# Performance work log

Hardware: AMD Instinct MI355X
Metric: run time of the kernel (lower is better)

The kernel has to match this reference:

```python
import jax, jax.numpy as jnp
import numpy as np

B, T, C, H = 4, 2048, 1024, 16
D = C // H  # head_dim = 64


def setup_inputs() -> dict:
    key = jax.random.key(0)
    ks = jax.random.split(key, 4)
    scale = 1.0 / np.sqrt(C)
    return {
        "x": jax.random.normal(ks[0], (B, T, C), dtype=jnp.float32),
        "attn_mask": jnp.ones((B, T), dtype=jnp.int32),
        "W_qkv": jax.random.normal(ks[1], (C, 3 * C), dtype=jnp.float32) * scale,
        "b_qkv": jnp.zeros((3 * C,), dtype=jnp.float32),
        "W_proj": jax.random.normal(ks[2], (C, C), dtype=jnp.float32) * scale,
        "b_proj": jnp.zeros((C,), dtype=jnp.float32),
    }


def reference(x, attn_mask, W_qkv, b_qkv, W_proj, b_proj):
    b, t, c = x.shape
    qkv = x @ W_qkv + b_qkv                      # (B,T,3C)
    q, k, v = jnp.split(qkv, 3, axis=-1)
    # b t (h d) -> b h t d
    q = q.reshape(b, t, H, D).transpose(0, 2, 1, 3)
    k = k.reshape(b, t, H, D).transpose(0, 2, 1, 3)
    v = v.reshape(b, t, H, D).transpose(0, 2, 1, 3)
    att = jnp.einsum("bhtd,bhsd->bhts", q, k) / jnp.sqrt(jnp.float32(D))
    causal = jnp.tril(jnp.ones((t, t), dtype=bool))[None, None]       # (1,1,T,T)
    pad = (attn_mask[:, None, None, :t] != 0)                         # (B,1,1,T)
    att = jnp.where(causal & pad, att, -jnp.inf)
    att = jax.nn.softmax(att, axis=-1)
    y = jnp.einsum("bhts,bhsd->bhtd", att, v)   # (B,H,T,D)
    y = y.transpose(0, 2, 1, 3).reshape(b, t, c)
    return y @ W_proj + b_proj
```

## Files before the change

kernel.cpp:

```cpp
#include <hip/hip_runtime.h>
#include <math.h>

#define B_ 4
#define T_ 2048
#define C_ 1024
#define H_ 16
#define D_ 64
#define M_ (B_*T_)
#define N1_ (3*C_)

typedef __attribute__((ext_vector_type(8))) short bf16x8;
typedef __attribute__((ext_vector_type(4))) short bf16x4;
typedef __attribute__((ext_vector_type(4))) float f32x4;
typedef __attribute__((ext_vector_type(16))) float f32x16;

__device__ __forceinline__ short f2bf(float f){
  union { float f; unsigned u; } v; v.f = f;
  unsigned r = (v.u + 0x7fffu + ((v.u >> 16) & 1u)) >> 16;
  return (short)r;
}

__device__ __forceinline__ unsigned cvtpk(float lo, float hi){
  unsigned r;
  asm("v_cvt_pk_bf16_f32 %0, %1, %2" : "=v"(r) : "v"(lo), "v"(hi));
  return r;
}

__device__ __forceinline__ void plswap(unsigned &a, unsigned &b){
  asm volatile("v_permlane32_swap_b32 %0, %1" : "+v"(a), "+v"(b));
}
__device__ __forceinline__ float xhalf_add(float x){
  unsigned a = __float_as_uint(x), b = a;
  asm volatile("v_permlane32_swap_b32 %0, %1" : "+v"(a), "+v"(b));
  return __uint_as_float(a) + __uint_as_float(b);
}

__device__ __forceinline__ void gll16(const void* g, void* l){
  __builtin_amdgcn_global_load_lds((const __attribute__((address_space(1))) void*)g,
                                   (__attribute__((address_space(3))) void*)l, 16, 0, 0);
}

__global__ __launch_bounds__(256) void convx(const float* __restrict__ x, short* __restrict__ xb, int n){
  int i = (blockIdx.x*256 + threadIdx.x)*8;
  if (i >= n) return;
  float4 a = *(const float4*)(x+i), b = *(const float4*)(x+i+4);
  bf16x8 o;
  o[0]=f2bf(a.x); o[1]=f2bf(a.y); o[2]=f2bf(a.z); o[3]=f2bf(a.w);
  o[4]=f2bf(b.x); o[5]=f2bf(b.y); o[6]=f2bf(b.z); o[7]=f2bf(b.w);
  *(bf16x8*)(xb+i) = o;
}

__global__ __launch_bounds__(256) void transw(const float* __restrict__ W, short* __restrict__ Wt, int K, int N){
  __shared__ float tl[64][72];
  int tid = threadIdx.x;
  int n0 = blockIdx.x*64, k0 = blockIdx.y*64;
  #pragma unroll
  for (int i=0;i<4;i++){
    int row = (tid>>4) + i*16;
    int col4 = (tid&15)*4;
    float4 v = *(const float4*)&W[(size_t)(k0+row)*N + n0 + col4];
    *(float4*)&tl[row][col4] = v;
  }
  __syncthreads();
  #pragma unroll
  for (int i=0;i<2;i++){
    int nr = (tid>>3) + i*32;
    int ch = tid&7;
    bf16x8 o;
    #pragma unroll
    for (int e=0;e<8;e++) o[e] = f2bf(tl[ch*8+e][nr]);
    *(bf16x8*)&Wt[(size_t)(n0+nr)*K + k0 + ch*8] = o;
  }
}

template<int OUTBF>
__global__ __launch_bounds__(512) void gemm_bt(const short* __restrict__ A, const short* __restrict__ Bt,
           const float* __restrict__ bias, short* __restrict__ outb, float* __restrict__ outf,
           int M, int N, int K)
{
  __shared__ __attribute__((aligned(128))) char LDSC[147456];
  const int tid = threadIdx.x;
  const int wv = tid>>6, ln = tid&63;
  const int lnr = ln&15, lg = ln>>4;
  const int wm = wv>>1, wn = wv&1;
  const int nx = gridDim.x;
  const int nwg = nx*gridDim.y;
  const int lin = blockIdx.x + nx*blockIdx.y;
  const int swz = (lin&7)*(nwg>>3) + (lin>>3);
  const int m0 = (swz/nx)*256, n0 = (swz%nx)*128;

  const int srA = tid>>3;
  const int sg  = (tid&7) ^ (srA&7);
  const short* Ag = A  + (size_t)(m0 + srA)*K + sg*8;
  const short* Bg = Bt + (size_t)(n0 + srA)*K + sg*8;

  const int fsw = (lg ^ (lnr&7))<<4;
  const int aln = (wm*64 + lnr)*128 + fsw;
  const int bln = (wn*64 + lnr)*128 + fsw;

  auto STAGE = [&](int kt, int bi){
    const short* a = Ag + kt*64;
    const short* b = Bg + kt*64;
    char* ab = LDSC + bi*32768 + wv*1024;
    char* bb = LDSC + 98304 + bi*16384 + wv*1024;
    gll16(a,                ab);
    gll16(a + (size_t)64*K, ab + 8192);
    gll16(a + (size_t)128*K, ab + 16384);
    gll16(a + (size_t)192*K, ab + 24576);
    gll16(b,                bb);
    gll16(b + (size_t)64*K, bb + 8192);
  };

  f32x4 acc[4][4];
  #pragma unroll
  for (int i=0;i<4;i++)
    #pragma unroll
    for (int j=0;j<4;j++) acc[i][j] = (f32x4){0.f,0.f,0.f,0.f};

  const int NT = K >> 6;
  STAGE(0, 0);
  STAGE(1, 1);
  asm volatile("s_waitcnt vmcnt(6)" ::: "memory");
  __builtin_amdgcn_sched_barrier(0);
  __builtin_amdgcn_s_barrier();
  __builtin_amdgcn_sched_barrier(0);

  int cb = 0, sb = 2;
  #pragma unroll 1
  for (int kt = 0; kt < NT; kt++){
    if (kt + 2 < NT) STAGE(kt + 2, sb);

    const char* ab = LDSC + cb*32768;
    const char* bb = LDSC + 98304 + cb*16384;
    bf16x8 af[4][2], bfr[4][2];
    #pragma unroll
    for (int mi=0;mi<4;mi++)
      #pragma unroll
      for (int ks=0;ks<2;ks++)
        af[mi][ks] = *(const bf16x8*)(ab + ((aln + mi*2048) ^ (ks<<6)));
    #pragma unroll
    for (int ni=0;ni<4;ni++)
      #pragma unroll
      for (int ks=0;ks<2;ks++)
        bfr[ni][ks] = *(const bf16x8*)(bb + ((bln + ni*2048) ^ (ks<<6)));

    __builtin_amdgcn_s_setprio(1);
    #pragma unroll
    for (int mi=0;mi<4;mi++)
      #pragma unroll
      for (int ni=0;ni<4;ni++)
        #pragma unroll
        for (int ks=0;ks<2;ks++)
          acc[mi][ni] = __builtin_amdgcn_mfma_f32_16x16x32_bf16(af[mi][ks], bfr[ni][ks], acc[mi][ni], 0,0,0);
    __builtin_amdgcn_s_setprio(0);

    if (kt < NT-1){
      __builtin_amdgcn_sched_barrier(0);
      if (kt < NT-2){ asm volatile("s_waitcnt vmcnt(6)" ::: "memory"); }
      else          { asm volatile("s_waitcnt vmcnt(0)" ::: "memory"); }
      __builtin_amdgcn_sched_barrier(0);
      __builtin_amdgcn_s_barrier();
      __builtin_amdgcn_sched_barrier(0);
    }
    cb = (cb==2) ? 0 : cb+1;
    sb = (sb==2) ? 0 : sb+1;
  }

  #pragma unroll
  for (int mi=0;mi<4;mi++){
    #pragma unroll
    for (int ni=0;ni<4;ni++){
      int col = n0 + wn*64 + ni*16 + lnr;
      float bv = bias[col];
      #pragma unroll
      for (int r=0;r<4;r++){
        int row = m0 + wm*64 + mi*16 + lg*4 + r;
        float v = acc[mi][ni][r] + bv;
        if (OUTBF) outb[(size_t)row*N + col] = f2bf(v);
        else       outf[(size_t)row*N + col] = v;
      }
    }
  }
}

__global__ __launch_bounds__(256) void transv(const short* __restrict__ qkv, short* __restrict__ vt){
  __shared__ short tl[64][72];
  int tid = threadIdx.x;
  int t0 = blockIdx.x*64, bh = blockIdx.y;
  int b = bh>>4, h = bh&15;
  int tr = tid>>2, cc = (tid&3)*16;
  const short* src = &qkv[(size_t)(b*T_ + t0 + tr)*N1_ + 2*C_ + h*D_ + cc];
  #pragma unroll
  for (int i=0;i<4;i++){
    bf16x4 v = *(const bf16x4*)(src + i*4);
    *(bf16x4*)&tl[tr][cc + i*4] = v;
  }
  __syncthreads();
  int d = tid>>2, tc = (tid&3)*16;
  #pragma unroll
  for (int i=0;i<2;i++){
    bf16x8 o;
    #pragma unroll
    for (int e=0;e<8;e++) o[e] = tl[tc + i*8 + e][d];
    *(bf16x8*)&vt[(size_t)(bh*D_ + d)*T_ + t0 + tc + i*8] = o;
  }
}

__global__ __launch_bounds__(256) void attn12(const short* __restrict__ qkv, const short* __restrict__ vt,
           const int* __restrict__ mask, short* __restrict__ yb)
{
  __shared__ short Ks[64*64];
  __shared__ short Vs[64*64];
  const int tid = threadIdx.x;
  const int wv = tid>>6, ln = tid&63;
  const int l31 = ln & 31, hi = ln >> 5;
  const int bh = blockIdx.x, b = bh>>4, hd = bh&15;
  const int c = 15 - (int)blockIdx.y;
  const float cexp = 0.18033688f;
  const float MC   = 11.541561f;

  const int srow = tid>>3;
  const int scol = (tid&7) ^ (srow&7);
  const short* kgb = qkv + (size_t)(b*T_ + srow)*N1_ + C_ + hd*D_ + scol*8;
  const short* vgb = vt  + (size_t)((bh<<6) + srow)*T_ + scol*8;
  int fa[4];
  #pragma unroll
  for (int i=0;i<4;i++)
    fa[i] = l31*128 + ((((i<<1)+hi) ^ (l31&7)) << 4);

  char* ksb = (char*)Ks;
  char* vsb = (char*)Vs;

  const int q0w = c*128 + wv*32;
  const int ntb  = 2*c + 2;
  const int myNt = 2*c + 1 + (wv>>1);

  bf16x8 qf[4];
  const short* qbase = qkv + (size_t)(b*T_ + q0w + l31)*N1_ + hd*D_ + hi*8;
  #pragma unroll
  for (int ds=0; ds<4; ds++) qf[ds] = *(const bf16x8*)(qbase + ds*16);

  f32x16 o0, o1;
  #pragma unroll
  for (int r=0;r<16;r++){ o0[r]=0.f; o1[r]=0.f; }
  float lsum = 0.f;

  #pragma unroll 1
  for (int jt = 0; jt < ntb; jt++){
    const int j0 = jt << 6;

    int mval = mask[b*T_ + j0 + ln];
    const short* kg = kgb + (size_t)j0*N1_;
    const short* vg = vgb + j0;
    gll16(kg,                    ksb + wv*1024);
    gll16(kg + (size_t)32*N1_,   ksb + 4096 + wv*1024);
    gll16(vg,                    vsb + wv*1024);
    gll16(vg + (size_t)32*T_,    vsb + 4096 + wv*1024);
    unsigned long long bm = __ballot(mval != 0);
    __syncthreads();

    if (jt < myNt){
      f32x16 s0, s1;
      #pragma unroll
      for (int r=0;r<16;r++){ s0[r]=0.f; s1[r]=0.f; }
      __builtin_amdgcn_s_setprio(1);
      #pragma unroll
      for (int ds=0; ds<4; ds++){
        bf16x8 k0 = *(const bf16x8*)(ksb + fa[ds]);
        bf16x8 k1 = *(const bf16x8*)(ksb + fa[ds] + 4096);
        s0 = __builtin_amdgcn_mfma_f32_32x32x16_bf16(k0, qf[ds], s0, 0,0,0);
        s1 = __builtin_amdgcn_mfma_f32_32x32x16_bf16(k1, qf[ds], s1, 0,0,0);
      }
      __builtin_amdgcn_s_setprio(0);

      const int qglob = q0w + l31;
      const bool allm = (bm == ~0ull);
      if (!allm){
        #pragma unroll
        for (int r=0;r<16;r++){
          int kr = (r&3) + 8*(r>>2) + 4*hi;
          bool ok0 = (j0 + kr      <= qglob) && ((bm >> kr) & 1);
          bool ok1 = (j0 + kr + 32 <= qglob) && ((bm >> (kr+32)) & 1);
          s0[r] = ok0 ? s0[r] : -INFINITY;
          s1[r] = ok1 ? s1[r] : -INFINITY;
        }
      } else if (j0 + 63 > q0w){
        #pragma unroll
        for (int r=0;r<16;r++){
          int kr = (r&3) + 8*(r>>2) + 4*hi;
          s0[r] = (j0 + kr      <= qglob) ? s0[r] : -INFINITY;
          s1[r] = (j0 + kr + 32 <= qglob) ? s1[r] : -INFINITY;
        }
      }

      #pragma unroll
      for (int r=0;r<16;r++){
        s0[r] = __builtin_amdgcn_exp2f(__builtin_fmaf(s0[r], cexp, -MC));
        s1[r] = __builtin_amdgcn_exp2f(__builtin_fmaf(s1[r], cexp, -MC));
      }
      float u[8];
      #pragma unroll
      for (int i=0;i<8;i++) u[i] = (s0[i]+s0[i+8]) + (s1[i]+s1[i+8]);
      #pragma unroll
      for (int i=0;i<4;i++) u[i] = u[i] + u[i+4];
      float ps = (u[0]+u[1]) + (u[2]+u[3]);
      lsum += xhalf_add(ps);

      unsigned LA[2][4], LB[2][4];
      #pragma unroll
      for (int rq=0; rq<4; rq++){
        LA[0][rq] = cvtpk(s0[4*rq],   s0[4*rq+1]);
        LB[0][rq] = cvtpk(s0[4*rq+2], s0[4*rq+3]);
        LA[1][rq] = cvtpk(s1[4*rq],   s1[4*rq+1]);
        LB[1][rq] = cvtpk(s1[4*rq+2], s1[4*rq+3]);
      }

      #pragma unroll
      for (int kt2=0; kt2<4; kt2++){
        const int kt = kt2>>1, sub = kt2&1;
        bf16x8 v0 = *(const bf16x8*)(vsb + fa[kt2]);
        bf16x8 v1 = *(const bf16x8*)(vsb + fa[kt2] + 4096);
        unsigned a0 = LA[kt][2*sub], a1 = LA[kt][2*sub+1];
        unsigned b0 = LB[kt][2*sub], b1 = LB[kt][2*sub+1];
        plswap(a0, a1);
        plswap(b0, b1);
        union { unsigned u[4]; bf16x8 v; } pf;
        pf.u[0] = a0; pf.u[1] = b0; pf.u[2] = a1; pf.u[3] = b1;
        __builtin_amdgcn_s_setprio(1);
        o0 = __builtin_amdgcn_mfma_f32_32x32x16_bf16(pf.v, v0, o0, 0,0,0);
        o1 = __builtin_amdgcn_mfma_f32_32x32x16_bf16(pf.v, v1, o1, 0,0,0);
        __builtin_amdgcn_s_setprio(0);
      }
    }
    __syncthreads();
  }

  float linv = 1.0f / lsum;
  #pragma unroll
  for (int r=0;r<16;r++){
    int qs = (r&3) + 8*(r>>2) + 4*hi;
    float lv = __shfl(linv, qs);
    size_t base = (size_t)(b*T_ + q0w + qs)*C_ + hd*D_ + l31;
    yb[base]      = f2bf(o0[r]*lv);
    yb[base + 32] = f2bf(o1[r]*lv);
  }
}

extern "C" void kernel_launch(void* const* d_in, const int* in_sizes, int n_in,
                              void* d_out, int out_size, void* d_ws, size_t ws_size,
                              hipStream_t stream){
  const float* x     = (const float*)d_in[0];
  const int*   mask  = (const int*)d_in[1];
  const float* Wqkv  = (const float*)d_in[2];
  const float* bqkv  = (const float*)d_in[3];
  const float* Wproj = (const float*)d_in[4];
  const float* bproj = (const float*)d_in[5];
  float* out = (float*)d_out;

  char* w = (char*)d_ws;
  short* xb     = (short*)w; w += (size_t)M_*C_*2;
  short* wqkvT  = (short*)w; w += (size_t)N1_*C_*2;
  short* wprojT = (short*)w; w += (size_t)C_*C_*2;
  short* qkvb   = (short*)w; w += (size_t)M_*N1_*2;
  short* vtb    = (short*)w; w += (size_t)B_*H_*D_*T_*2;
  short* yb     = (short*)w; w += (size_t)M_*C_*2;

  convx<<<dim3((M_*C_)/(256*8)), 256, 0, stream>>>(x, xb, M_*C_);
  transw<<<dim3(N1_/64, C_/64), 256, 0, stream>>>(Wqkv, wqkvT, C_, N1_);
  transw<<<dim3(C_/64,  C_/64), 256, 0, stream>>>(Wproj, wprojT, C_, C_);
  gemm_bt<1><<<dim3(N1_/128, M_/256), 512, 0, stream>>>(xb, wqkvT, bqkv, qkvb, nullptr, M_, N1_, C_);
  transv<<<dim3(T_/64, B_*H_), 256, 0, stream>>>(qkvb, vtb);
  attn12<<<dim3(B_*H_, 16), 256, 0, stream>>>(qkvb, vtb, mask, yb);
  gemm_bt<0><<<dim3(C_/128, M_/256), 512, 0, stream>>>(yb, wprojT, bproj, nullptr, out, M_, C_, C_);
}
```

Measured before the change: 181.2 us.

## Fuse V transpose and Q scaling into QKV GEMM epilogue, drop transv kernel

The QKV GEMM epilogue now writes the V part straight into the transposed per-head layout and pre-scales Q by the softmax exponent constant, so the separate transv kernel and its launch are removed. The attention kernel starts its score accumulators at -MC and applies exp2 directly, dropping one FMA per score. The cost is that the transposed V stores from the epilogue are scattered, with a stride of T elements between neighbouring columns, and Q now carries an extra bf16 rounding after scaling.

```diff
diff --git a/kernel.cpp b/kernel.cpp
--- a/kernel.cpp
+++ b/kernel.cpp
@@ -76,7 +76,7 @@
 template<int OUTBF>
 __global__ __launch_bounds__(512) void gemm_bt(const short* __restrict__ A, const short* __restrict__ Bt,
            const float* __restrict__ bias, short* __restrict__ outb, float* __restrict__ outf,
-           int M, int N, int K)
+           short* __restrict__ vtb, int M, int N, int K)
 {
   __shared__ __attribute__((aligned(128))) char LDSC[147456];
   const int tid = threadIdx.x;
@@ -176,37 +176,24 @@
       for (int r=0;r<4;r++){
         int row = m0 + wm*64 + mi*16 + lg*4 + r;
         float v = acc[mi][ni][r] + bv;
-        if (OUTBF) outb[(size_t)row*N + col] = f2bf(v);
-        else       outf[(size_t)row*N + col] = v;
+        if (OUTBF){
+          if (col >= 2*C_){
+            int cc = col - 2*C_;
+            int bb2 = row >> 11, tt = row & (T_-1);
+            vtb[((size_t)((bb2*H_ + (cc>>6))*D_ + (cc&63)))*T_ + tt] = f2bf(v);
+          } else {
+            if (col < C_) v *= 0.18033688f;
+            outb[(size_t)row*N + col] = f2bf(v);
+          }
+        } else {
+          outf[(size_t)row*N + col] = v;
+        }
       }
     }
   }
 }
 
-__global__ __launch_bounds__(256) void transv(const short* __restrict__ qkv, short* __restrict__ vt){
-  __shared__ short tl[64][72];
-  int tid = threadIdx.x;
-  int t0 = blockIdx.x*64, bh = blockIdx.y;
-  int b = bh>>4, h = bh&15;
-  int tr = tid>>2, cc = (tid&3)*16;
-  const short* src = &qkv[(size_t)(b*T_ + t0 + tr)*N1_ + 2*C_ + h*D_ + cc];
-  #pragma unroll
-  for (int i=0;i<4;i++){
-    bf16x4 v = *(const bf16x4*)(src + i*4);
-    *(bf16x4*)&tl[tr][cc + i*4] = v;
-  }
-  __syncthreads();
-  int d = tid>>2, tc = (tid&3)*16;
-  #pragma unroll
-  for (int i=0;i<2;i++){
-    bf16x8 o;
-    #pragma unroll
-    for (int e=0;e<8;e++) o[e] = tl[tc + i*8 + e][d];
-    *(bf16x8*)&vt[(size_t)(bh*D_ + d)*T_ + t0 + tc + i*8] = o;
-  }
-}
-
-__global__ __launch_bounds__(256) void attn12(const short* __restrict__ qkv, const short* __restrict__ vt,
+__global__ __launch_bounds__(256) void attn14(const short* __restrict__ qkv, const short* __restrict__ vt,
            const int* __restrict__ mask, short* __restrict__ yb)
 {
   __shared__ short Ks[64*64];
@@ -216,8 +203,7 @@
   const int l31 = ln & 31, hi = ln >> 5;
   const int bh = blockIdx.x, b = bh>>4, hd = bh&15;
   const int c = 15 - (int)blockIdx.y;
-  const float cexp = 0.18033688f;
-  const float MC   = 11.541561f;
+  const float MC = 11.541561f;
 
   const int srow = tid>>3;
   const int scol = (tid&7) ^ (srow&7);
@@ -262,7 +248,7 @@
     if (jt < myNt){
       f32x16 s0, s1;
       #pragma unroll
-      for (int r=0;r<16;r++){ s0[r]=0.f; s1[r]=0.f; }
+      for (int r=0;r<16;r++){ s0[r]=-MC; s1[r]=-MC; }
       __builtin_amdgcn_s_setprio(1);
       #pragma unroll
       for (int ds=0; ds<4; ds++){
@@ -295,8 +281,8 @@
 
       #pragma unroll
       for (int r=0;r<16;r++){
-        s0[r] = __builtin_amdgcn_exp2f(__builtin_fmaf(s0[r], cexp, -MC));
-        s1[r] = __builtin_amdgcn_exp2f(__builtin_fmaf(s1[r], cexp, -MC));
+        s0[r] = __builtin_amdgcn_exp2f(s0[r]);
+        s1[r] = __builtin_amdgcn_exp2f(s1[r]);
       }
       float u[8];
       #pragma unroll
@@ -368,8 +354,7 @@
   convx<<<dim3((M_*C_)/(256*8)), 256, 0, stream>>>(x, xb, M_*C_);
   transw<<<dim3(N1_/64, C_/64), 256, 0, stream>>>(Wqkv, wqkvT, C_, N1_);
   transw<<<dim3(C_/64,  C_/64), 256, 0, stream>>>(Wproj, wprojT, C_, C_);
-  gemm_bt<1><<<dim3(N1_/128, M_/256), 512, 0, stream>>>(xb, wqkvT, bqkv, qkvb, nullptr, M_, N1_, C_);
-  transv<<<dim3(T_/64, B_*H_), 256, 0, stream>>>(qkvb, vtb);
-  attn12<<<dim3(B_*H_, 16), 256, 0, stream>>>(qkvb, vtb, mask, yb);
-  gemm_bt<0><<<dim3(C_/128, M_/256), 512, 0, stream>>>(yb, wprojT, bproj, nullptr, out, M_, C_, C_);
-}
+  gemm_bt<1><<<dim3(N1_/128, M_/256), 512, 0, stream>>>(xb, wqkvT, bqkv, qkvb, nullptr, vtb, M_, N1_, C_);
+  attn14<<<dim3(B_*H_, 16), 256, 0, stream>>>(qkvb, vtb, mask, yb);
+  gemm_bt<0><<<dim3(C_/128, M_/256), 512, 0, stream>>>(yb, wprojT, bproj, nullptr, out, nullptr, M_, C_, C_);
+}
```

Measured after the change: 185.8 us. +2.6%, slower.
